# Kernel tuning notes

Hardware: AMD Instinct MI355X
Metric: run time of the kernel (lower is better)

## Reference

```python
import jax, jax.numpy as jnp
import numpy as np

C = 768            # config.channels
CH, CW = 16, 16    # coarse span shape for group 'screen'
N = CH * CW        # total coarse positions = 256
FH, FW, FP = 16, 16, 2
F = FH * FW * FP   # fine_total = 512
K = 4              # top4 sample mode
B = 1024           # sb


def _ln(x, g, b, eps=1e-5):
    m = jnp.mean(x, axis=-1, keepdims=True)
    v = jnp.mean((x - m) ** 2, axis=-1, keepdims=True)
    return (x - m) / jnp.sqrt(v + eps) * g + b


def _mlp3(x, W1, b1, W2, b2, W3, b3):
    h = jax.nn.gelu(x @ W1 + b1)
    h = jax.nn.gelu(h @ W2 + b2)
    return h @ W3 + b3


def setup_inputs() -> dict:
    key = jax.random.key(0)
    ks = jax.random.split(key, 16)

    def w(k, fan_in, shape):
        return jax.random.normal(k, shape, jnp.float32) * (1.0 / np.sqrt(fan_in))

    return {
        "x": jax.random.normal(ks[0], (B, C), jnp.float32),
        "g_in": jnp.ones((C,), jnp.float32),
        "b_in": jnp.zeros((C,), jnp.float32),
        # coarse head: C -> C -> C -> N
        "cW1": w(ks[1], C, (C, C)), "cb1": jnp.zeros((C,), jnp.float32),
        "cW2": w(ks[2], C, (C, C)), "cb2": jnp.zeros((C,), jnp.float32),
        "cW3": w(ks[3], C, (C, N)), "cb3": jnp.zeros((N,), jnp.float32),
        # coarse embedding
        "emb": jax.random.normal(ks[4], (N, C), jnp.float32),
        "g_e": jnp.ones((C,), jnp.float32),
        "b_e": jnp.zeros((C,), jnp.float32),
        # fine head: 2C -> C -> C -> F
        "fW1": w(ks[5], 2 * C, (2 * C, C)), "fb1": jnp.zeros((C,), jnp.float32),
        "fW2": w(ks[6], C, (C, C)), "fb2": jnp.zeros((C,), jnp.float32),
        "fW3": w(ks[7], C, (C, F)), "fb3": jnp.zeros((F,), jnp.float32),
        # no-op head
        "nW": w(ks[8], C, (C, 1)), "nb": jnp.zeros((1,), jnp.float32),
    }


def reference(x, g_in, b_in, cW1, cb1, cW2, cb2, cW3, cb3, emb, g_e, b_e,
              fW1, fb1, fW2, fb2, fW3, fb3, nW, nb):
    b = x.shape[0]
    xn = _ln(x, g_in, b_in)                                   # (b, C)
    no_op = xn @ nW + nb                                      # (b, 1)
    coarse = _mlp3(xn, cW1, cb1, cW2, cb2, cW3, cb3)          # (b, N)

    # top4 routing
    _, i = jax.lax.top_k(coarse, K)                           # (b, K) int32
    e = _ln(emb[i], g_e, b_e)                                 # (b, K, C)
    fine_in = jnp.concatenate(
        [jnp.broadcast_to(xn[:, None, :], (b, K, C)), e], axis=-1)  # (b, K, 2C)
    fine = _mlp3(fine_in, fW1, fb1, fW2, fb2, fW3, fb3)       # (b, K, F)

    log_f = jnp.log(jnp.float32(F))
    xfull = jnp.broadcast_to(coarse[:, :, None], (b, N, F)) - log_f  # (b, N, F)
    upd = fine + log_f - jax.nn.logsumexp(fine, axis=-1, keepdims=True)
    xfull = xfull.at[jnp.arange(b)[:, None], i].add(upd)      # scatter-combine

    # per-group permute: (b, ch, cw, fh, fw, fp) -> (b, ch, fh, cw, fw, fp)
    xg = xfull.reshape(b, CH, CW, FH, FW, FP)
    xg = jnp.transpose(xg, (0, 1, 3, 2, 4, 5)).reshape(b, -1)
    return jnp.concatenate([no_op, xg], axis=-1)              # (b, 1 + N*F)
```

## Files before the change

### kernel.cpp

```cpp
#include <hip/hip_runtime.h>
#include <hip/hip_bf16.h>
#include <math.h>

typedef unsigned short u16;
typedef unsigned int   u32;
typedef __attribute__((ext_vector_type(8))) short s16x8;
typedef __attribute__((ext_vector_type(4))) short s16x4;
typedef __attribute__((ext_vector_type(4))) float f32x4;

#define CB 768
#define NB 256
#define FB 512
#define BATCH 1024
#define OUTC 131073
#define LOGF 6.2383246250395077f

__device__ __forceinline__ u16 f2bf(float f){
    u32 u = __float_as_uint(f);
    u32 r = u + 0x7FFFu + ((u >> 16) & 1u);
    return (u16)(r >> 16);
}
__device__ __forceinline__ float bf2f(u16 s){ return __uint_as_float(((u32)s) << 16); }
__device__ __forceinline__ bool probe_bf(const void* g){ return ((const u16*)g)[0] == 0x3F80u; }
__device__ __forceinline__ float loadraw(const void* p, size_t i, bool isbf){
    return isbf ? bf2f(((const u16*)p)[i]) : ((const float*)p)[i];
}
__device__ __forceinline__ void split3(float f, u16& h, u16& l, u16& q){
    h = f2bf(f); float r1 = f - bf2f(h);
    l = f2bf(r1); float r2 = r1 - bf2f(l);
    q = f2bf(r2);
}
__device__ __forceinline__ float gelu_f(float x){
    return 0.5f * x * (1.0f + tanhf(0.7978845608028654f * (x + 0.044715f * x * x * x)));
}
__device__ __forceinline__ f32x4 mfma16x16x32(s16x8 a, s16x8 b, f32x4 c){
    return __builtin_amdgcn_mfma_f32_16x16x32_bf16(a, b, c, 0, 0, 0);
}

template<int W> struct VecT;
template<> struct VecT<4>{ using T = s16x4; };
template<> struct VecT<8>{ using T = s16x8; };

__device__ __forceinline__ float blockReduce(float v, float* sb, bool domax){
    #pragma unroll
    for (int o = 32; o > 0; o >>= 1){
        float ov = __shfl_down(v, o, 64);
        v = domax ? fmaxf(v, ov) : (v + ov);
    }
    int w = threadIdx.x >> 6, lane = threadIdx.x & 63;
    if (lane == 0) sb[w] = v;
    __syncthreads();
    float r = domax ? fmaxf(fmaxf(sb[0], sb[1]), fmaxf(sb[2], sb[3]))
                    : (sb[0] + sb[1] + sb[2] + sb[3]);
    __syncthreads();
    return r;
}

struct TransDesc { const void* src; u16* dh; u16* dl; int K; int N; int start; int tilesX; };
struct TD6 { TransDesc d[6]; };

#define T_TRANS   3456
#define T_LNX_END 4480
#define T_LEM_END 4736
#define T_CI_END  4752
#define T_KS_END  4768
#define T_GRID    4769

__global__ __launch_bounds__(256) void prep_k(TD6 td,
        const void* x, const void* g, const void* bb, const void* nW, const void* nb,
        const void* emb, const void* ge, const void* be, const void* cb3, const void* ginp,
        u16* __restrict__ xh, u16* __restrict__ xl, u16* __restrict__ xq,
        u16* __restrict__ lnemb, float* __restrict__ noop,
        float* __restrict__ coarse, unsigned char* __restrict__ ksel,
        float* __restrict__ sumexp){
    __shared__ float t[32][33];
    __shared__ float sb[4];
    bool isbf = probe_bf(ginp);
    int blk = blockIdx.x, tid = threadIdx.x;
    if (blk < T_TRANS){
        int e = 0;
        #pragma unroll
        for (int i = 1; i < 6; i++) if (blk >= td.d[i].start) e = i;
        TransDesc d = td.d[e];
        int rel = blk - d.start;
        int n0 = (rel % d.tilesX) * 32;
        int k0 = (rel / d.tilesX) * 32;
        int tx = tid & 31, ty = tid >> 5;
        #pragma unroll
        for (int i = 0; i < 32; i += 8)
            t[ty + i][tx] = loadraw(d.src, (size_t)(k0 + ty + i) * d.N + n0 + tx, isbf);
        __syncthreads();
        #pragma unroll
        for (int i = 0; i < 32; i += 8){
            float f = t[tx][ty + i];
            u16 h = f2bf(f);
            d.dh[(size_t)(n0 + ty + i) * d.K + k0 + tx] = h;
            if (d.dl)
                d.dl[(size_t)(n0 + ty + i) * d.K + k0 + tx] = f2bf(f - bf2f(h));
        }
    } else if (blk < T_LNX_END){
        int b = blk - T_TRANS;
        float v[3];
        #pragma unroll
        for (int i = 0; i < 3; i++) v[i] = loadraw(x, (size_t)b * CB + tid + i * 256, isbf);
        float mean = blockReduce(v[0] + v[1] + v[2], sb, false) * (1.0f / 768.0f);
        float d0 = v[0] - mean, d1 = v[1] - mean, d2 = v[2] - mean;
        float var = blockReduce(d0*d0 + d1*d1 + d2*d2, sb, false) * (1.0f / 768.0f);
        float inv = 1.0f / sqrtf(var + 1e-5f);
        float dot = 0.0f;
        #pragma unroll
        for (int i = 0; i < 3; i++){
            int c = tid + i * 256;
            float xi = (v[i] - mean) * inv * loadraw(g, c, isbf) + loadraw(bb, c, isbf);
            u16 h, l, q; split3(xi, h, l, q);
            size_t o = (size_t)b * CB + c;
            xh[o] = h; xl[o] = l; xq[o] = q;
            dot += xi * loadraw(nW, c, isbf);
        }
        dot = blockReduce(dot, sb, false);
        if (tid == 0) noop[b] = dot + loadraw(nb, 0, isbf);
    } else if (blk < T_LEM_END){
        int n = blk - T_LNX_END;
        float v[3];
        #pragma unroll
        for (int i = 0; i < 3; i++) v[i] = loadraw(emb, (size_t)n * CB + tid + i * 256, isbf);
        float mean = blockReduce(v[0] + v[1] + v[2], sb, false) * (1.0f / 768.0f);
        float d0 = v[0] - mean, d1 = v[1] - mean, d2 = v[2] - mean;
        float var = blockReduce(d0*d0 + d1*d1 + d2*d2, sb, false) * (1.0f / 768.0f);
        float inv = 1.0f / sqrtf(var + 1e-5f);
        #pragma unroll
        for (int i = 0; i < 3; i++){
            int c = tid + i * 256;
            lnemb[(size_t)n * CB + c] =
                f2bf((v[i] - mean) * inv * loadraw(ge, c, isbf) + loadraw(be, c, isbf));
        }
    } else if (blk < T_CI_END){
        int base = (blk - T_LEM_END) * 16384;
        #pragma unroll
        for (int j = 0; j < 64; j++){
            int i = base + j * 256 + tid;
            coarse[i] = loadraw(cb3, i & 255, isbf);
        }
    } else if (blk < T_KS_END){
        int base = (blk - T_CI_END) * 4096;
        u32* kp = (u32*)ksel;
        #pragma unroll
        for (int j = 0; j < 16; j++) kp[base + j * 256 + tid] = 0xFFFFFFFFu;
    } else {
        #pragma unroll
        for (int j = 0; j < 16; j++) sumexp[j * 256 + tid] = 0.0f;
    }
}

template<int ASPLIT, int BSPLIT, int ACT, int OUTMODE, int TM, int TN, int GATHER>
__global__ __launch_bounds__(512) void gemm_k(
        const u16* __restrict__ Ah, const u16* __restrict__ Al, const u16* __restrict__ Aq,
        const int* __restrict__ gidx,
        const u16* __restrict__ Bth, const u16* __restrict__ Btl,
        const void* __restrict__ bias, const void* __restrict__ ginp,
        void* __restrict__ o0, void* __restrict__ o1, void* __restrict__ o2,
        int M, int N, int K, int lda, int ldb){
    constexpr int LDA = 40;
    constexpr int MT = TM / 32;
    constexpr int NT = TN / 64;
    constexpr int AW = TM / 16;
    constexpr int BW = TN / 16;
    using AV = typename VecT<AW>::T;
    using BV = typename VecT<BW>::T;
    __shared__ u16 As[ASPLIT][TM * LDA];
    __shared__ u16 Bs[BSPLIT][TN * LDA];
    bool isbf = probe_bf(ginp);
    const int m0 = blockIdx.y * TM, n0 = blockIdx.x * TN;
    const int tid = threadIdx.x;
    const int w = tid >> 6, lane = tid & 63, lm = lane & 15, q = lane >> 4;
    const int wr = w & 1, wc = w >> 1;
    const int kc = K / gridDim.z;
    const int kbeg = blockIdx.z * kc, kend = kbeg + kc;
    f32x4 acc[MT][NT];
    #pragma unroll
    for (int i = 0; i < MT; i++)
        #pragma unroll
        for (int j = 0; j < NT; j++) acc[i][j] = (f32x4)(0.0f);
    const int ar = tid / (32 / AW);
    const int ac = (tid % (32 / AW)) * AW;
    const int bn = tid / (32 / BW);
    const int bc = (tid % (32 / BW)) * BW;
    const u16* Apl[3] = { Ah, Al, Aq };
    const u16* Bpl[2] = { Bth, Btl };
    const int arow = GATHER ? gidx[m0 + ar] : (m0 + ar);

    AV pa[ASPLIT]; BV pb[BSPLIT];
    auto load_regs = [&](int kk){
        #pragma unroll
        for (int s = 0; s < ASPLIT; s++)
            pa[s] = *(const AV*)(Apl[s] + (size_t)arow * lda + kk + ac);
        #pragma unroll
        for (int s = 0; s < BSPLIT; s++)
            pb[s] = *(const BV*)(Bpl[s] + (size_t)(n0 + bn) * ldb + kk + bc);
    };

    load_regs(kbeg);
    for (int k0 = kbeg; k0 < kend; k0 += 32){
        __syncthreads();
        #pragma unroll
        for (int s = 0; s < ASPLIT; s++)
            *(AV*)&As[s][ar*LDA + ac] = pa[s];
        #pragma unroll
        for (int s = 0; s < BSPLIT; s++)
            *(BV*)&Bs[s][bn*LDA + bc] = pb[s];
        __syncthreads();
        if (k0 + 32 < kend) load_regs(k0 + 32);

        s16x8 afr[ASPLIT][MT], bfr[BSPLIT][NT];
        #pragma unroll
        for (int mt = 0; mt < MT; mt++)
            #pragma unroll
            for (int s = 0; s < ASPLIT; s++)
                afr[s][mt] = *(const s16x8*)&As[s][((mt*2 + wr)*16 + lm)*LDA + q*8];
        #pragma unroll
        for (int nt = 0; nt < NT; nt++)
            #pragma unroll
            for (int s = 0; s < BSPLIT; s++)
                bfr[s][nt] = *(const s16x8*)&Bs[s][((nt*4 + wc)*16 + lm)*LDA + q*8];
        #pragma unroll
        for (int mt = 0; mt < MT; mt++)
            #pragma unroll
            for (int nt = 0; nt < NT; nt++){
                acc[mt][nt] = mfma16x16x32(afr[0][mt], bfr[0][nt], acc[mt][nt]);
                if (ASPLIT == 3){
                    acc[mt][nt] = mfma16x16x32(afr[1][mt], bfr[0][nt], acc[mt][nt]);
                    acc[mt][nt] = mfma16x16x32(afr[2][mt], bfr[0][nt], acc[mt][nt]);
                }
                if (BSPLIT == 2){
                    acc[mt][nt] = mfma16x16x32(afr[0][mt], bfr[1][nt], acc[mt][nt]);
                    if (ASPLIT == 3)
                        acc[mt][nt] = mfma16x16x32(afr[1][mt], bfr[1][nt], acc[mt][nt]);
                }
            }
    }

    if (OUTMODE == 3){
        #pragma unroll
        for (int nt = 0; nt < NT; nt++){
            int n = n0 + (nt*4 + wc)*16 + lm;
            #pragma unroll
            for (int mt = 0; mt < MT; mt++)
                #pragma unroll
                for (int r = 0; r < 4; r++){
                    int m = m0 + (mt*2 + wr)*16 + q*4 + r;
                    atomicAdd(&((float*)o0)[(size_t)m * N + n], acc[mt][nt][r]);
                }
        }
    } else if (OUTMODE == 4){
        #pragma unroll
        for (int mt = 0; mt < MT; mt++)
            #pragma unroll
            for (int r = 0; r < 4; r++){
                int m = m0 + (mt*2 + wr)*16 + q*4 + r;
                float esum = 0.0f;
                #pragma unroll
                for (int nt = 0; nt < NT; nt++){
                    int n = n0 + (nt*4 + wc)*16 + lm;
                    float vv = acc[mt][nt][r] + (bias ? loadraw(bias, n, isbf) : 0.0f);
                    ((float*)o0)[(size_t)m * N + n] = vv;
                    esum += expf(vv);
                }
                #pragma unroll
                for (int o = 8; o > 0; o >>= 1) esum += __shfl_down(esum, o, 16);
                if (lm == 0) atomicAdd(&((float*)o1)[m], esum);
            }
    } else if (OUTMODE == 5){
        #pragma unroll
        for (int nt = 0; nt < NT; nt++){
            int n = n0 + (nt*4 + wc)*16 + lm;
            float bv = bias ? loadraw(bias, n, isbf) : 0.0f;
            #pragma unroll
            for (int mt = 0; mt < MT; mt++){
                #pragma unroll
                for (int r = 0; r < 4; r++){
                    int m = m0 + (mt*2 + wr)*16 + q*4 + r;
                    float xv = ((const float*)o1)[(size_t)(m >> 2) * N + n];
                    ((u16*)o0)[(size_t)m * N + n] = f2bf(gelu_f(acc[mt][nt][r] + bv + xv));
                }
            }
        }
    } else {
        #pragma unroll
        for (int nt = 0; nt < NT; nt++){
            int n = n0 + (nt*4 + wc)*16 + lm;
            float bv = bias ? loadraw(bias, n, isbf) : 0.0f;
            #pragma unroll
            for (int mt = 0; mt < MT; mt++){
                #pragma unroll
                for (int r = 0; r < 4; r++){
                    int m = m0 + (mt*2 + wr)*16 + q*4 + r;
                    float vv = acc[mt][nt][r] + bv;
                    if (ACT == 1) vv = gelu_f(vv);
                    size_t o = (size_t)m * N + n;
                    if (OUTMODE == 0)      ((float*)o0)[o] = vv;
                    else if (OUTMODE == 1) ((u16*)o0)[o] = f2bf(vv);
                    else {
                        u16 h, l, qq; split3(vv, h, l, qq);
                        ((u16*)o0)[o] = h; ((u16*)o1)[o] = l; ((u16*)o2)[o] = qq;
                    }
                }
            }
        }
    }
}

__global__ __launch_bounds__(256) void topk_k(const float* __restrict__ coarse,
        int* __restrict__ idx, unsigned char* __restrict__ ksel){
    int w = threadIdx.x >> 6, lane = threadIdx.x & 63;
    int b = blockIdx.x * 4 + w;
    const float* cr = coarse + (size_t)b * NB;
    float v[4]; int id[4];
    #pragma unroll
    for (int j = 0; j < 4; j++){ id[j] = lane + 64*j; v[j] = cr[id[j]]; }
    for (int k = 0; k < 4; k++){
        float bv = v[0]; int bi = id[0];
        #pragma unroll
        for (int j = 1; j < 4; j++)
            if (v[j] > bv || (v[j] == bv && id[j] < bi)){ bv = v[j]; bi = id[j]; }
        #pragma unroll
        for (int o = 32; o > 0; o >>= 1){
            float ov = __shfl_xor(bv, o, 64);
            int   oi = __shfl_xor(bi, o, 64);
            if (ov > bv || (ov == bv && oi < bi)){ bv = ov; bi = oi; }
        }
        if (lane == 0){ idx[b*4 + k] = bi; ksel[(size_t)b * NB + bi] = (unsigned char)k; }
        #pragma unroll
        for (int j = 0; j < 4; j++) if (id[j] == bi) v[j] = -INFINITY;
    }
}

__global__ __launch_bounds__(256) void out_k(const float* __restrict__ coarse,
        const float* __restrict__ fine, const float* __restrict__ sumexp,
        const unsigned char* __restrict__ ksel, const float* __restrict__ noop,
        const void* __restrict__ ginp, void* __restrict__ outp){
    u32 g0 = ((u32)blockIdx.x * 256u + (u32)threadIdx.x) * 8u;
    const u32 total = (u32)BATCH * (u32)OUTC;
    if (g0 >= total) return;
    bool isbf = probe_bf(ginp);
    u32 qq = g0 >> 17;
    int rr = (int)(g0 & 131071u) - (int)qq;
    if (rr < 0){ qq -= 1u; rr += 131073; }
    int b = (int)qq;
    int lastkey = -1, ks = 255, fr = 0;
    float cv = 0.0f, lbase = 0.0f;
    float vals[8];
    #pragma unroll
    for (int e = 0; e < 8; e++){
        float val;
        if (rr == 0){
            val = noop[b];
        } else {
            int j = rr - 1;
            int n = ((j >> 13) << 4) | ((j >> 5) & 15);
            int key = (b << 8) | n;
            if (key != lastkey){
                lastkey = key;
                size_t o = (size_t)b * NB + n;
                cv = coarse[o] - LOGF;
                ks = ksel[o];
                if (ks != 255){
                    fr = b * 4 + ks;
                    lbase = LOGF - logf(sumexp[fr]);
                }
            }
            val = cv;
            if (ks != 255)
                val += fine[((size_t)fr << 9) + (((j >> 9) & 15) << 5) + (j & 31)] + lbase;
        }
        vals[e] = val;
        rr++;
        if (rr == 131073){ rr = 0; b++; }
    }
    if (isbf){
        u16 res[8];
        #pragma unroll
        for (int e = 0; e < 8; e++) res[e] = f2bf(vals[e]);
        *(s16x8*)((u16*)outp + g0) = *(s16x8*)res;
    } else {
        float* of = (float*)outp + g0;
        *(float4*)(of)     = make_float4(vals[0], vals[1], vals[2], vals[3]);
        *(float4*)(of + 4) = make_float4(vals[4], vals[5], vals[6], vals[7]);
    }
}

extern "C" void kernel_launch(void* const* d_in, const int* in_sizes, int n_in,
                              void* d_out, int out_size, void* d_ws, size_t ws_size,
                              hipStream_t stream){
    (void)in_sizes; (void)n_in; (void)out_size; (void)ws_size;
    char* ws = (char*)d_ws;
    size_t off = 0;
    auto alloc = [&](size_t bytes){ void* p = ws + off; off += (bytes + 255) & ~(size_t)255; return p; };

    u16* xh  = (u16*)alloc((size_t)1024*768*2);
    u16* xl  = (u16*)alloc((size_t)1024*768*2);
    u16* xq  = (u16*)alloc((size_t)1024*768*2);
    u16* h1h = (u16*)alloc((size_t)1024*768*2);
    u16* h1l = (u16*)alloc((size_t)1024*768*2);
    u16* h1q = (u16*)alloc((size_t)1024*768*2);
    u16* h2h = (u16*)alloc((size_t)1024*768*2);
    u16* h2l = (u16*)alloc((size_t)1024*768*2);
    u16* h2q = (u16*)alloc((size_t)1024*768*2);
    u16* lnemb = (u16*)alloc((size_t)256*768*2);
    float* coarse = (float*)alloc((size_t)1024*256*4);
    unsigned char* ksel = (unsigned char*)alloc((size_t)1024*256);
    float* noop   = (float*)alloc((size_t)1024*4);
    float* sumexp = (float*)alloc((size_t)4096*4);
    int*   idx    = (int*)alloc((size_t)4096*4);
    float* xpart  = (float*)alloc((size_t)1024*768*4);
    u16*   gg1    = (u16*)  alloc((size_t)4096*768*2);
    u16*   gg2    = (u16*)  alloc((size_t)4096*768*2);
    float* fine   = (float*)alloc((size_t)4096*512*4);
    u16* cW1th = (u16*)alloc((size_t)768*768*2);
    u16* cW1tl = (u16*)alloc((size_t)768*768*2);
    u16* cW2th = (u16*)alloc((size_t)768*768*2);
    u16* cW2tl = (u16*)alloc((size_t)768*768*2);
    u16* cW3th = (u16*)alloc((size_t)768*256*2);
    u16* cW3tl = (u16*)alloc((size_t)768*256*2);
    u16* fW1t  = (u16*)alloc((size_t)768*1536*2);
    u16* fW2t  = (u16*)alloc((size_t)768*768*2);
    u16* fW3t  = (u16*)alloc((size_t)512*768*2);

    const void* ginp = d_in[1];

    TD6 td;
    td.d[0] = { d_in[3],  cW1th, cW1tl,  768, 768,    0, 24 };
    td.d[1] = { d_in[5],  cW2th, cW2tl,  768, 768,  576, 24 };
    td.d[2] = { d_in[7],  cW3th, cW3tl,  768, 256, 1152,  8 };
    td.d[3] = { d_in[12], fW1t,  nullptr,1536, 768, 1344, 24 };
    td.d[4] = { d_in[14], fW2t,  nullptr, 768, 768, 2496, 24 };
    td.d[5] = { d_in[16], fW3t,  nullptr, 768, 512, 3072, 16 };

    prep_k<<<T_GRID, 256, 0, stream>>>(td, d_in[0], d_in[1], d_in[2], d_in[18], d_in[19],
            d_in[9], d_in[10], d_in[11], d_in[8], ginp,
            xh, xl, xq, lnemb, noop, coarse, ksel, sumexp);

    gemm_k<1,1,0,0,128,128,0><<<dim3(6, 8, 1), 512, 0, stream>>>(
            xh, nullptr, nullptr, nullptr, fW1t, nullptr,
            nullptr, ginp, xpart, nullptr, nullptr, 1024, 768, 768, 768, 1536);

    gemm_k<3,2,1,2,64,64,0><<<dim3(12, 16, 1), 512, 0, stream>>>(
            xh, xl, xq, nullptr, cW1th, cW1tl,
            d_in[4], ginp, h1h, h1l, h1q, 1024, 768, 768, 768, 768);
    gemm_k<3,2,1,2,64,64,0><<<dim3(12, 16, 1), 512, 0, stream>>>(
            h1h, h1l, h1q, nullptr, cW2th, cW2tl,
            d_in[6], ginp, h2h, h2l, h2q, 1024, 768, 768, 768, 768);
    gemm_k<3,2,0,3,64,64,0><<<dim3( 4, 16, 3), 512, 0, stream>>>(
            h2h, h2l, h2q, nullptr, cW3th, cW3tl,
            nullptr, ginp, coarse, nullptr, nullptr, 1024, 256, 768, 768, 768);

    topk_k<<<256, 256, 0, stream>>>(coarse, idx, ksel);

    gemm_k<1,1,0,5,128,128,1><<<dim3(6, 32, 1), 512, 0, stream>>>(
            lnemb, nullptr, nullptr, idx, fW1t + 768, nullptr,
            d_in[13], ginp, gg1, xpart, nullptr, 4096, 768, 768, 768, 1536);
    gemm_k<1,1,1,1,128,128,0><<<dim3(6, 32, 1), 512, 0, stream>>>(
            gg1, nullptr, nullptr, nullptr, fW2t, nullptr,
            d_in[15], ginp, gg2, nullptr, nullptr, 4096, 768, 768, 768, 768);
    gemm_k<1,1,0,4,128,128,0><<<dim3(4, 32, 1), 512, 0, stream>>>(
            gg2, nullptr, nullptr, nullptr, fW3t, nullptr,
            d_in[17], ginp, fine, sumexp, nullptr, 4096, 512, 768, 768, 768);

    u32 total_chunks = ((u32)BATCH * (u32)OUTC) / 8u;
    u32 blocks = (total_chunks + 255u) / 256u;
    out_k<<<blocks, 256, 0, stream>>>(coarse, fine, sumexp, ksel, noop, ginp, d_out);
}
```

Before: 755.6 us.

## Deepen GEMM K-tile to 64, fuse first two GEMMs, retune tiles and occupancy

The GEMM body now stages 64-wide K slices in shared memory (padded stride 72) with 16-byte vector loads, which halves the number of barrier pairs per K loop. The x·fW1 partial GEMM and the first coarse layer are merged into a single launch with heterogeneous blocks. The fine-head GEMMs switch to 64x128 tiles with a minimum-occupancy hint, doubling their block count, and the coarse output GEMM uses a 4-way K split instead of 3. The aim is to cut launch count, synchronisation overhead and under-filled grids, at the cost of more shared memory per block and more atomics in the split-K output.

```diff
diff --git a/kernel.cpp b/kernel.cpp
--- a/kernel.cpp
+++ b/kernel.cpp
@@ -5,7 +5,6 @@
 typedef unsigned short u16;
 typedef unsigned int   u32;
 typedef __attribute__((ext_vector_type(8))) short s16x8;
-typedef __attribute__((ext_vector_type(4))) short s16x4;
 typedef __attribute__((ext_vector_type(4))) float f32x4;
 
 #define CB 768
@@ -36,10 +35,6 @@
 __device__ __forceinline__ f32x4 mfma16x16x32(s16x8 a, s16x8 b, f32x4 c){
     return __builtin_amdgcn_mfma_f32_16x16x32_bf16(a, b, c, 0, 0, 0);
 }
-
-template<int W> struct VecT;
-template<> struct VecT<4>{ using T = s16x4; };
-template<> struct VecT<8>{ using T = s16x8; };
 
 __device__ __forceinline__ float blockReduce(float v, float* sb, bool domax){
     #pragma unroll
@@ -153,90 +148,98 @@
 }
 
 template<int ASPLIT, int BSPLIT, int ACT, int OUTMODE, int TM, int TN, int GATHER>
-__global__ __launch_bounds__(512) void gemm_k(
+__device__ __forceinline__ void gemm_body(u16* sm,
         const u16* __restrict__ Ah, const u16* __restrict__ Al, const u16* __restrict__ Aq,
         const int* __restrict__ gidx,
         const u16* __restrict__ Bth, const u16* __restrict__ Btl,
-        const void* __restrict__ bias, const void* __restrict__ ginp,
+        const void* __restrict__ bias, bool isbf,
         void* __restrict__ o0, void* __restrict__ o1, void* __restrict__ o2,
-        int M, int N, int K, int lda, int ldb){
-    constexpr int LDA = 40;
+        int bx, int by, int kbeg, int kend, int N, int lda, int ldb){
+    constexpr int LDA = 72;
     constexpr int MT = TM / 32;
     constexpr int NT = TN / 64;
-    constexpr int AW = TM / 16;
-    constexpr int BW = TN / 16;
-    using AV = typename VecT<AW>::T;
-    using BV = typename VecT<BW>::T;
-    __shared__ u16 As[ASPLIT][TM * LDA];
-    __shared__ u16 Bs[BSPLIT][TN * LDA];
-    bool isbf = probe_bf(ginp);
-    const int m0 = blockIdx.y * TM, n0 = blockIdx.x * TN;
+    constexpr int AC = TM / 64;
+    constexpr int BC = TN / 64;
+    u16* As = sm;
+    u16* Bs = sm + ASPLIT * TM * LDA;
+    const int m0 = by * TM, n0 = bx * TN;
     const int tid = threadIdx.x;
     const int w = tid >> 6, lane = tid & 63, lm = lane & 15, q = lane >> 4;
     const int wr = w & 1, wc = w >> 1;
-    const int kc = K / gridDim.z;
-    const int kbeg = blockIdx.z * kc, kend = kbeg + kc;
     f32x4 acc[MT][NT];
     #pragma unroll
     for (int i = 0; i < MT; i++)
         #pragma unroll
         for (int j = 0; j < NT; j++) acc[i][j] = (f32x4)(0.0f);
-    const int ar = tid / (32 / AW);
-    const int ac = (tid % (32 / AW)) * AW;
-    const int bn = tid / (32 / BW);
-    const int bc = (tid % (32 / BW)) * BW;
+    const int ar = (AC == 2) ? (tid >> 2) : (tid >> 3);
+    const int ac = (AC == 2) ? ((tid & 3) * 16) : ((tid & 7) * 8);
+    const int bn = (BC == 2) ? (tid >> 2) : (tid >> 3);
+    const int bc = (BC == 2) ? ((tid & 3) * 16) : ((tid & 7) * 8);
     const u16* Apl[3] = { Ah, Al, Aq };
     const u16* Bpl[2] = { Bth, Btl };
     const int arow = GATHER ? gidx[m0 + ar] : (m0 + ar);
 
-    AV pa[ASPLIT]; BV pb[BSPLIT];
+    s16x8 pa[ASPLIT][AC], pb[BSPLIT][BC];
     auto load_regs = [&](int kk){
         #pragma unroll
-        for (int s = 0; s < ASPLIT; s++)
-            pa[s] = *(const AV*)(Apl[s] + (size_t)arow * lda + kk + ac);
-        #pragma unroll
-        for (int s = 0; s < BSPLIT; s++)
-            pb[s] = *(const BV*)(Bpl[s] + (size_t)(n0 + bn) * ldb + kk + bc);
+        for (int s = 0; s < ASPLIT; s++){
+            const u16* sp = Apl[s] + (size_t)arow * lda + kk + ac;
+            pa[s][0] = *(const s16x8*)(sp);
+            if (AC == 2) pa[s][1] = *(const s16x8*)(sp + 8);
+        }
+        #pragma unroll
+        for (int s = 0; s < BSPLIT; s++){
+            const u16* sp = Bpl[s] + (size_t)(n0 + bn) * ldb + kk + bc;
+            pb[s][0] = *(const s16x8*)(sp);
+            if (BC == 2) pb[s][1] = *(const s16x8*)(sp + 8);
+        }
     };
 
     load_regs(kbeg);
-    for (int k0 = kbeg; k0 < kend; k0 += 32){
+    for (int k0 = kbeg; k0 < kend; k0 += 64){
         __syncthreads();
         #pragma unroll
-        for (int s = 0; s < ASPLIT; s++)
-            *(AV*)&As[s][ar*LDA + ac] = pa[s];
-        #pragma unroll
-        for (int s = 0; s < BSPLIT; s++)
-            *(BV*)&Bs[s][bn*LDA + bc] = pb[s];
+        for (int s = 0; s < ASPLIT; s++){
+            *(s16x8*)&As[s*TM*LDA + ar*LDA + ac] = pa[s][0];
+            if (AC == 2) *(s16x8*)&As[s*TM*LDA + ar*LDA + ac + 8] = pa[s][1];
+        }
+        #pragma unroll
+        for (int s = 0; s < BSPLIT; s++){
+            *(s16x8*)&Bs[s*TN*LDA + bn*LDA + bc] = pb[s][0];
+            if (BC == 2) *(s16x8*)&Bs[s*TN*LDA + bn*LDA + bc + 8] = pb[s][1];
+        }
         __syncthreads();
-        if (k0 + 32 < kend) load_regs(k0 + 32);
-
-        s16x8 afr[ASPLIT][MT], bfr[BSPLIT][NT];
-        #pragma unroll
-        for (int mt = 0; mt < MT; mt++)
-            #pragma unroll
-            for (int s = 0; s < ASPLIT; s++)
-                afr[s][mt] = *(const s16x8*)&As[s][((mt*2 + wr)*16 + lm)*LDA + q*8];
-        #pragma unroll
-        for (int nt = 0; nt < NT; nt++)
-            #pragma unroll
-            for (int s = 0; s < BSPLIT; s++)
-                bfr[s][nt] = *(const s16x8*)&Bs[s][((nt*4 + wc)*16 + lm)*LDA + q*8];
-        #pragma unroll
-        for (int mt = 0; mt < MT; mt++)
-            #pragma unroll
-            for (int nt = 0; nt < NT; nt++){
-                acc[mt][nt] = mfma16x16x32(afr[0][mt], bfr[0][nt], acc[mt][nt]);
-                if (ASPLIT == 3){
-                    acc[mt][nt] = mfma16x16x32(afr[1][mt], bfr[0][nt], acc[mt][nt]);
-                    acc[mt][nt] = mfma16x16x32(afr[2][mt], bfr[0][nt], acc[mt][nt]);
+        if (k0 + 64 < kend) load_regs(k0 + 64);
+
+        #pragma unroll
+        for (int kk = 0; kk < 2; kk++){
+            s16x8 afr[ASPLIT][MT], bfr[BSPLIT][NT];
+            #pragma unroll
+            for (int mt = 0; mt < MT; mt++)
+                #pragma unroll
+                for (int s = 0; s < ASPLIT; s++)
+                    afr[s][mt] = *(const s16x8*)&As[s*TM*LDA + ((mt*2 + wr)*16 + lm)*LDA + kk*32 + q*8];
+            #pragma unroll
+            for (int nt = 0; nt < NT; nt++)
+                #pragma unroll
+                for (int s = 0; s < BSPLIT; s++)
+                    bfr[s][nt] = *(const s16x8*)&Bs[s*TN*LDA + ((nt*4 + wc)*16 + lm)*LDA + kk*32 + q*8];
+            #pragma unroll
+            for (int mt = 0; mt < MT; mt++)
+                #pragma unroll
+                for (int nt = 0; nt < NT; nt++){
+                    acc[mt][nt] = mfma16x16x32(afr[0][mt], bfr[0][nt], acc[mt][nt]);
+                    if (ASPLIT == 3){
+                        acc[mt][nt] = mfma16x16x32(afr[1][mt], bfr[0][nt], acc[mt][nt]);
+                        acc[mt][nt] = mfma16x16x32(afr[2][mt], bfr[0][nt], acc[mt][nt]);
+                    }
+                    if (BSPLIT == 2){
+                        acc[mt][nt] = mfma16x16x32(afr[0][mt], bfr[1][nt], acc[mt][nt]);
+                        if (ASPLIT == 3)
+                            acc[mt][nt] = mfma16x16x32(afr[1][mt], bfr[1][nt], acc[mt][nt]);
+                    }
                 }
-                if (BSPLIT == 2){
-                    acc[mt][nt] = mfma16x16x32(afr[0][mt], bfr[1][nt], acc[mt][nt]);
-                    if (ASPLIT == 3)
-                        acc[mt][nt] = mfma16x16x32(afr[1][mt], bfr[1][nt], acc[mt][nt]);
-                }
-            }
+        }
     }
 
     if (OUTMODE == 3){
@@ -306,6 +309,43 @@
                 }
             }
         }
+    }
+}
+
+template<int ASPLIT, int BSPLIT, int ACT, int OUTMODE, int TM, int TN, int GATHER, int MINW>
+__global__ __launch_bounds__(512, MINW) void gemm_k(
+        const u16* __restrict__ Ah, const u16* __restrict__ Al, const u16* __restrict__ Aq,
+        const int* __restrict__ gidx,
+        const u16* __restrict__ Bth, const u16* __restrict__ Btl,
+        const void* __restrict__ bias, const void* __restrict__ ginp,
+        void* __restrict__ o0, void* __restrict__ o1, void* __restrict__ o2,
+        int K, int N, int lda, int ldb){
+    __shared__ u16 sm[(ASPLIT * TM + BSPLIT * TN) * 72];
+    bool isbf = probe_bf(ginp);
+    const int kc = K / gridDim.z;
+    const int kbeg = blockIdx.z * kc;
+    gemm_body<ASPLIT, BSPLIT, ACT, OUTMODE, TM, TN, GATHER>(sm,
+        Ah, Al, Aq, gidx, Bth, Btl, bias, isbf, o0, o1, o2,
+        blockIdx.x, blockIdx.y, kbeg, kbeg + kc, N, lda, ldb);
+}
+
+__global__ __launch_bounds__(512, 2) void c1x_k(
+        const u16* __restrict__ xh, const u16* __restrict__ xl, const u16* __restrict__ xq,
+        const u16* __restrict__ cW1th, const u16* __restrict__ cW1tl,
+        const void* __restrict__ cb1, const void* __restrict__ ginp,
+        u16* __restrict__ h1h, u16* __restrict__ h1l, u16* __restrict__ h1q,
+        const u16* __restrict__ fW1t, float* __restrict__ xpart){
+    __shared__ u16 sm[(3 * 64 + 2 * 64) * 72];
+    bool isbf = probe_bf(ginp);
+    if (blockIdx.x < 192){
+        gemm_body<3, 2, 1, 2, 64, 64, 0>(sm, xh, xl, xq, nullptr, cW1th, cW1tl,
+            cb1, isbf, h1h, h1l, h1q, blockIdx.x % 12, blockIdx.x / 12, 0, 768,
+            768, 768, 768);
+    } else {
+        int rel = blockIdx.x - 192;
+        gemm_body<1, 1, 0, 0, 128, 128, 0>(sm, xh, nullptr, nullptr, nullptr, fW1t, nullptr,
+            nullptr, isbf, xpart, nullptr, nullptr, rel % 6, rel / 6, 0, 768,
+            768, 768, 1536);
     }
 }
 
@@ -439,31 +479,27 @@
             d_in[9], d_in[10], d_in[11], d_in[8], ginp,
             xh, xl, xq, lnemb, noop, coarse, ksel, sumexp);
 
-    gemm_k<1,1,0,0,128,128,0><<<dim3(6, 8, 1), 512, 0, stream>>>(
-            xh, nullptr, nullptr, nullptr, fW1t, nullptr,
-            nullptr, ginp, xpart, nullptr, nullptr, 1024, 768, 768, 768, 1536);
-
-    gemm_k<3,2,1,2,64,64,0><<<dim3(12, 16, 1), 512, 0, stream>>>(
-            xh, xl, xq, nullptr, cW1th, cW1tl,
-            d_in[4], ginp, h1h, h1l, h1q, 1024, 768, 768, 768, 768);
-    gemm_k<3,2,1,2,64,64,0><<<dim3(12, 16, 1), 512, 0, stream>>>(
+    c1x_k<<<dim3(240, 1, 1), 512, 0, stream>>>(
+            xh, xl, xq, cW1th, cW1tl, d_in[4], ginp, h1h, h1l, h1q, fW1t, xpart);
+
+    gemm_k<3,2,1,2,64,64,0,2><<<dim3(12, 16, 1), 512, 0, stream>>>(
             h1h, h1l, h1q, nullptr, cW2th, cW2tl,
-            d_in[6], ginp, h2h, h2l, h2q, 1024, 768, 768, 768, 768);
-    gemm_k<3,2,0,3,64,64,0><<<dim3( 4, 16, 3), 512, 0, stream>>>(
+            d_in[6], ginp, h2h, h2l, h2q, 768, 768, 768, 768);
+    gemm_k<3,2,0,3,64,64,0,2><<<dim3(4, 16, 4), 512, 0, stream>>>(
             h2h, h2l, h2q, nullptr, cW3th, cW3tl,
-            nullptr, ginp, coarse, nullptr, nullptr, 1024, 256, 768, 768, 768);
+            nullptr, ginp, coarse, nullptr, nullptr, 768, 256, 768, 768);
 
     topk_k<<<256, 256, 0, stream>>>(coarse, idx, ksel);
 
-    gemm_k<1,1,0,5,128,128,1><<<dim3(6, 32, 1), 512, 0, stream>>>(
+    gemm_k<1,1,0,5,64,128,1,4><<<dim3(6, 64, 1), 512, 0, stream>>>(
             lnemb, nullptr, nullptr, idx, fW1t + 768, nullptr,
-            d_in[13], ginp, gg1, xpart, nullptr, 4096, 768, 768, 768, 1536);
-    gemm_k<1,1,1,1,128,128,0><<<dim3(6, 32, 1), 512, 0, stream>>>(
+            d_in[13], ginp, gg1, xpart, nullptr, 768, 768, 768, 1536);
+    gemm_k<1,1,1,1,64,128,0,4><<<dim3(6, 64, 1), 512, 0, stream>>>(
             gg1, nullptr, nullptr, nullptr, fW2t, nullptr,
-            d_in[15], ginp, gg2, nullptr, nullptr, 4096, 768, 768, 768, 768);
-    gemm_k<1,1,0,4,128,128,0><<<dim3(4, 32, 1), 512, 0, stream>>>(
+            d_in[15], ginp, gg2, nullptr, nullptr, 768, 768, 768, 768);
+    gemm_k<1,1,0,4,64,128,0,4><<<dim3(4, 64, 1), 512, 0, stream>>>(
             gg2, nullptr, nullptr, nullptr, fW3t, nullptr,
-            d_in[17], ginp, fine, sumexp, nullptr, 4096, 512, 768, 768, 768);
+            d_in[17], ginp, fine, sumexp, nullptr, 768, 512, 768, 768);
 
     u32 total_chunks = ((u32)BATCH * (u32)OUTC) / 8u;
     u32 blocks = (total_chunks + 255u) / 256u;
```

After: 714.5 us. 1.06x faster.
